# Kernel tuning notes

Measured on AMD Instinct MI355X. Metric: run time of the kernel, lower is better.

Reference implementation:

```python
import jax, jax.numpy as jnp
import numpy as np
from jax import lax

B, C, D, H, W = 2, 64, 64, 96, 96
HID = 8  # max(C // 8, 8)
NEG_SLOPE = 0.01  # torch LeakyReLU default


def setup_inputs() -> dict:
    key = jax.random.key(0)
    k_x, k_dw, k_f1w, k_f1b, k_f2w, k_f2b = jax.random.split(key, 6)
    x = jax.random.normal(k_x, (B, C, D, H, W), dtype=jnp.float32)
    # depthwise 3x3x3 kernel, OIDHW with I = C/groups = 1
    dw_w = jax.random.normal(k_dw, (C, 1, 3, 3, 3), dtype=jnp.float32) * 0.2
    fc1_w = jax.random.normal(k_f1w, (HID, C), dtype=jnp.float32) * 0.1
    fc1_b = jax.random.normal(k_f1b, (HID,), dtype=jnp.float32) * 0.1
    fc2_w = jax.random.normal(k_f2w, (C, HID), dtype=jnp.float32) * 0.1
    fc2_b = jax.random.normal(k_f2b, (C,), dtype=jnp.float32) * 0.1
    return {"x": x, "dw_w": dw_w, "fc1_w": fc1_w, "fc1_b": fc1_b,
            "fc2_w": fc2_w, "fc2_b": fc2_b}


def reference(x, dw_w, fc1_w, fc1_b, fc2_w, fc2_b):
    # depthwise 3x3x3 conv, padding=1, groups=C
    s = lax.conv_general_dilated(
        x, dw_w,
        window_strides=(1, 1, 1),
        padding=[(1, 1), (1, 1), (1, 1)],
        dimension_numbers=("NCDHW", "OIDHW", "NCDHW"),
        feature_group_count=C,
    )
    # squeeze: global average pool over D,H,W -> [B, C]
    z = s.mean(axis=(2, 3, 4))
    # excitation MLP (1x1x1 convs on [B,C,1,1,1] == dense layers on [B,C])
    h = jnp.einsum("bc,hc->bh", z, fc1_w) + fc1_b
    h = jnp.where(h >= 0, h, NEG_SLOPE * h)  # LeakyReLU(0.01)
    w = jax.nn.sigmoid(jnp.einsum("bh,ch->bc", h, fc2_w) + fc2_b)
    # broadcast channel gate
    return x * w[:, :, None, None, None]
```

## Files before the change

### kernel.cpp

```cpp
#include <hip/hip_runtime.h>
#include <math.h>

#define B 2
#define C 64
#define DD 64
#define HH 96
#define WW 96
#define HID 8
#define BC (B * C)
#define SLICE (HH * WW)
#define SLICE4 (SLICE / 4)
#define CHAN (DD * SLICE)
#define CHAN4 (CHAN / 4)
#define ROW4 (WW / 4)

#define RED_BX 16
#define DPB (DD / RED_BX)
#define SC_F4 16
#define SC_BX (CHAN4 / (256 * SC_F4))

#define WS_PART 0
#define WS_GATE (BC * RED_BX)

typedef float f4 __attribute__((ext_vector_type(4)));

__device__ __forceinline__ void compute_clsw(const float* __restrict__ dw_w,
                                             int c, int tid, float* w27) {
    if (tid < 27) {
        int cd = tid / 9, r = tid % 9, ch = r / 3, cw = r % 3;
        int kd0 = (cd == 2) ? 1 : 0, kd1 = (cd == 0) ? 1 : 2;
        int kh0 = (ch == 2) ? 1 : 0, kh1 = (ch == 0) ? 1 : 2;
        int kw0 = (cw == 2) ? 1 : 0, kw1 = (cw == 0) ? 1 : 2;
        float s = 0.f;
        for (int kd = kd0; kd <= kd1; ++kd)
            for (int kh = kh0; kh <= kh1; ++kh)
                for (int kw = kw0; kw <= kw1; ++kw)
                    s += dw_w[c * 27 + kd * 9 + kh * 3 + kw];
        w27[tid] = s;
    }
}

__global__ __launch_bounds__(256) void reduce_kernel(const float* __restrict__ x,
                                                     const float* __restrict__ dw_w,
                                                     float* __restrict__ ws) {
    const int bc = blockIdx.y;
    const int c  = bc & (C - 1);
    const int d0 = blockIdx.x * DPB;
    const int tid = threadIdx.x;

    __shared__ float w27[27];
    __shared__ float part[4];

    compute_clsw(dw_w, c, tid, w27);
    __syncthreads();

    const f4* xb = (const f4*)x + (size_t)bc * CHAN4;
    float acc = 0.f;

    const int h0 = tid / ROW4;
    const int j0 = tid - h0 * ROW4;

    for (int sd = 0; sd < DPB; ++sd) {
        const int d  = d0 + sd;
        const float* w9 = &w27[((d == 0) ? 0 : ((d == DD - 1) ? 2 : 1)) * 9];
        const f4* x4 = xb + (size_t)d * SLICE4;
        int h = h0, j = j0;
        #pragma unroll
        for (int it = 0; it < SLICE4 / 256; ++it) {
            f4 v = x4[it * 256 + tid];
            int chc = (h == 0) ? 0 : ((h == HH - 1) ? 2 : 1);
            float wmid = w9[chc * 3 + 1];
            float w0 = (j == 0) ? w9[chc * 3 + 0] : wmid;
            float w3 = (j == ROW4 - 1) ? w9[chc * 3 + 2] : wmid;
            acc += v.x * w0 + (v.y + v.z) * wmid + v.w * w3;
            h += 10; j += 16;
            if (j >= ROW4) { j -= ROW4; h += 1; }
        }
    }

    for (int off = 32; off > 0; off >>= 1)
        acc += __shfl_down(acc, off, 64);
    if ((tid & 63) == 0) part[tid >> 6] = acc;
    __syncthreads();
    if (tid == 0)
        ws[WS_PART + bc * RED_BX + blockIdx.x] = part[0] + part[1] + part[2] + part[3];
}

__global__ void gate_kernel(const float* __restrict__ fc1_w, const float* __restrict__ fc1_b,
                            const float* __restrict__ fc2_w, const float* __restrict__ fc2_b,
                            float* __restrict__ ws) {
    __shared__ float zsh[BC];
    __shared__ float hsh[B * HID];
    int t = threadIdx.x;
    float s0 = 0.f;
    for (int p = 0; p < RED_BX; ++p) s0 += ws[WS_PART + t * RED_BX + p];
    zsh[t] = s0 * (1.0f / (float)CHAN);
    __syncthreads();
    if (t < B * HID) {
        int b = t >> 3, j = t & 7;
        float s = fc1_b[j];
        for (int cc = 0; cc < C; ++cc) s += fc1_w[j * C + cc] * zsh[b * C + cc];
        hsh[t] = (s >= 0.f) ? s : 0.01f * s;
    }
    __syncthreads();
    int b = t >> 6, cc = t & (C - 1);
    float s = fc2_b[cc];
    for (int j = 0; j < HID; ++j) s += fc2_w[cc * HID + j] * hsh[b * HID + j];
    ws[WS_GATE + t] = 1.f / (1.f + expf(-s));
}

__global__ __launch_bounds__(256) void scale_kernel(const float* __restrict__ x,
                                                    const float* __restrict__ ws,
                                                    float* __restrict__ out) {
    const int bc = (BC - 1) - blockIdx.y;
    const int bx = (SC_BX - 1) - blockIdx.x;
    const float g = ws[WS_GATE + bc];
    const size_t base = (size_t)bc * CHAN4 + (size_t)bx * (256 * SC_F4) + threadIdx.x;
    const f4* xp = (const f4*)x;
    f4* op = (f4*)out;
    #pragma unroll
    for (int k = 0; k < SC_F4; ++k) {
        size_t idx = base + (size_t)k * 256;
        op[idx] = xp[idx] * g;
    }
}

extern "C" void kernel_launch(void* const* d_in, const int* in_sizes, int n_in,
                              void* d_out, int out_size, void* d_ws, size_t ws_size,
                              hipStream_t stream) {
    const float* x     = (const float*)d_in[0];
    const float* dw_w  = (const float*)d_in[1];
    const float* fc1_w = (const float*)d_in[2];
    const float* fc1_b = (const float*)d_in[3];
    const float* fc2_w = (const float*)d_in[4];
    const float* fc2_b = (const float*)d_in[5];
    float* out = (float*)d_out;
    float* ws  = (float*)d_ws;

    reduce_kernel<<<dim3(RED_BX, BC), dim3(256), 0, stream>>>(x, dw_w, ws);
    gate_kernel<<<dim3(1), dim3(BC), 0, stream>>>(fc1_w, fc1_b, fc2_w, fc2_b, ws);
    scale_kernel<<<dim3(SC_BX, BC), dim3(256), 0, stream>>>(x, ws, out);
}
```

Before: 558.0 us.

## Fuse gate MLP into scale kernel and restructure reduction loop for interior chunks

Removes the separate single-block gate kernel. Each scale block now recomputes the channel's gate from the partial sums, which saves one launch and the serialization gap between kernels. The reduction kernel gains a fast path for interior depth chunks: per-position weights are precomputed once and reused across four depth slices, with four independent accumulators to raise memory-level parallelism. The trade-off is redundant MLP work in every scale block, plus the dropped reversed block ordering that previously aimed for cache reuse of x.

```diff
diff --git a/kernel.cpp b/kernel.cpp
--- a/kernel.cpp
+++ b/kernel.cpp
@@ -13,6 +13,7 @@
 #define CHAN (DD * SLICE)
 #define CHAN4 (CHAN / 4)
 #define ROW4 (WW / 4)
+#define SEGS (SLICE4 / 256)
 
 #define RED_BX 16
 #define DPB (DD / RED_BX)
@@ -20,7 +21,6 @@
 #define SC_BX (CHAN4 / (256 * SC_F4))
 
 #define WS_PART 0
-#define WS_GATE (BC * RED_BX)
 
 typedef float f4 __attribute__((ext_vector_type(4)));
 
@@ -43,79 +43,110 @@
 __global__ __launch_bounds__(256) void reduce_kernel(const float* __restrict__ x,
                                                      const float* __restrict__ dw_w,
                                                      float* __restrict__ ws) {
-    const int bc = blockIdx.y;
-    const int c  = bc & (C - 1);
-    const int d0 = blockIdx.x * DPB;
-    const int tid = threadIdx.x;
+    const int bc    = blockIdx.y;
+    const int c     = bc & (C - 1);
+    const int chunk = blockIdx.x;
+    const int d0    = chunk * DPB;
+    const int tid   = threadIdx.x;
 
     __shared__ float w27[27];
     __shared__ float part[4];
-
     compute_clsw(dw_w, c, tid, w27);
     __syncthreads();
 
-    const f4* xb = (const f4*)x + (size_t)bc * CHAN4;
-    float acc = 0.f;
+    const f4* xb = (const f4*)x + (size_t)bc * CHAN4 + (size_t)d0 * SLICE4;
+    float acc[DPB] = {0.f, 0.f, 0.f, 0.f};
 
-    const int h0 = tid / ROW4;
-    const int j0 = tid - h0 * ROW4;
-
-    for (int sd = 0; sd < DPB; ++sd) {
-        const int d  = d0 + sd;
-        const float* w9 = &w27[((d == 0) ? 0 : ((d == DD - 1) ? 2 : 1)) * 9];
-        const f4* x4 = xb + (size_t)d * SLICE4;
-        int h = h0, j = j0;
+    if (chunk != 0 && chunk != RED_BX - 1) {
+        float w0r[SEGS], wmr[SEGS], w3r[SEGS];
         #pragma unroll
-        for (int it = 0; it < SLICE4 / 256; ++it) {
-            f4 v = x4[it * 256 + tid];
+        for (int s = 0; s < SEGS; ++s) {
+            int p = s * 256 + tid;
+            int h = p / ROW4;
+            int j = p - h * ROW4;
             int chc = (h == 0) ? 0 : ((h == HH - 1) ? 2 : 1);
-            float wmid = w9[chc * 3 + 1];
-            float w0 = (j == 0) ? w9[chc * 3 + 0] : wmid;
-            float w3 = (j == ROW4 - 1) ? w9[chc * 3 + 2] : wmid;
-            acc += v.x * w0 + (v.y + v.z) * wmid + v.w * w3;
-            h += 10; j += 16;
-            if (j >= ROW4) { j -= ROW4; h += 1; }
+            float wm = w27[9 + chc * 3 + 1];
+            wmr[s] = wm;
+            w0r[s] = (j == 0)        ? w27[9 + chc * 3 + 0] : wm;
+            w3r[s] = (j == ROW4 - 1) ? w27[9 + chc * 3 + 2] : wm;
+        }
+        #pragma unroll
+        for (int s = 0; s < SEGS; ++s) {
+            const int p = s * 256 + tid;
+            #pragma unroll
+            for (int sd = 0; sd < DPB; ++sd) {
+                f4 v = xb[(size_t)sd * SLICE4 + p];
+                acc[sd] += v.x * w0r[s] + (v.y + v.z) * wmr[s] + v.w * w3r[s];
+            }
+        }
+    } else {
+        #pragma unroll
+        for (int sd = 0; sd < DPB; ++sd) {
+            const int d  = d0 + sd;
+            const int cd = (d == 0) ? 0 : ((d == DD - 1) ? 2 : 1);
+            #pragma unroll
+            for (int s = 0; s < SEGS; ++s) {
+                int p = s * 256 + tid;
+                int h = p / ROW4;
+                int j = p - h * ROW4;
+                int chc = (h == 0) ? 0 : ((h == HH - 1) ? 2 : 1);
+                float wm = w27[cd * 9 + chc * 3 + 1];
+                float w0 = (j == 0)        ? w27[cd * 9 + chc * 3 + 0] : wm;
+                float w3 = (j == ROW4 - 1) ? w27[cd * 9 + chc * 3 + 2] : wm;
+                f4 v = xb[(size_t)sd * SLICE4 + p];
+                acc[sd] += v.x * w0 + (v.y + v.z) * wm + v.w * w3;
+            }
         }
     }
 
+    float a = (acc[0] + acc[1]) + (acc[2] + acc[3]);
     for (int off = 32; off > 0; off >>= 1)
-        acc += __shfl_down(acc, off, 64);
-    if ((tid & 63) == 0) part[tid >> 6] = acc;
+        a += __shfl_down(a, off, 64);
+    if ((tid & 63) == 0) part[tid >> 6] = a;
     __syncthreads();
     if (tid == 0)
-        ws[WS_PART + bc * RED_BX + blockIdx.x] = part[0] + part[1] + part[2] + part[3];
+        ws[WS_PART + bc * RED_BX + chunk] = (part[0] + part[1]) + (part[2] + part[3]);
 }
 
-__global__ void gate_kernel(const float* __restrict__ fc1_w, const float* __restrict__ fc1_b,
-                            const float* __restrict__ fc2_w, const float* __restrict__ fc2_b,
-                            float* __restrict__ ws) {
-    __shared__ float zsh[BC];
-    __shared__ float hsh[B * HID];
-    int t = threadIdx.x;
-    float s0 = 0.f;
-    for (int p = 0; p < RED_BX; ++p) s0 += ws[WS_PART + t * RED_BX + p];
-    zsh[t] = s0 * (1.0f / (float)CHAN);
+__global__ __launch_bounds__(256) void scale_kernel(
+        const float* __restrict__ x,
+        const float* __restrict__ fc1_w, const float* __restrict__ fc1_b,
+        const float* __restrict__ fc2_w, const float* __restrict__ fc2_b,
+        const float* __restrict__ ws, float* __restrict__ out) {
+    const int bc = blockIdx.y;
+    const int b  = bc >> 6;
+    const int c  = bc & (C - 1);
+    const int t  = threadIdx.x;
+
+    __shared__ float zsh[C];
+    __shared__ float hsh[HID];
+    __shared__ float gsh;
+
+    if (t < C) {
+        float s0 = 0.f;
+        #pragma unroll
+        for (int p = 0; p < RED_BX; ++p)
+            s0 += ws[WS_PART + (b * C + t) * RED_BX + p];
+        zsh[t] = s0 * (1.0f / (float)CHAN);
+    }
     __syncthreads();
-    if (t < B * HID) {
-        int b = t >> 3, j = t & 7;
-        float s = fc1_b[j];
-        for (int cc = 0; cc < C; ++cc) s += fc1_w[j * C + cc] * zsh[b * C + cc];
+    if (t < HID) {
+        float s = fc1_b[t];
+        #pragma unroll
+        for (int cc = 0; cc < C; ++cc) s += fc1_w[t * C + cc] * zsh[cc];
         hsh[t] = (s >= 0.f) ? s : 0.01f * s;
     }
     __syncthreads();
-    int b = t >> 6, cc = t & (C - 1);
-    float s = fc2_b[cc];
-    for (int j = 0; j < HID; ++j) s += fc2_w[cc * HID + j] * hsh[b * HID + j];
-    ws[WS_GATE + t] = 1.f / (1.f + expf(-s));
-}
+    if (t == 0) {
+        float s = fc2_b[c];
+        #pragma unroll
+        for (int j = 0; j < HID; ++j) s += fc2_w[c * HID + j] * hsh[j];
+        gsh = 1.f / (1.f + expf(-s));
+    }
+    __syncthreads();
+    const float g = gsh;
 
-__global__ __launch_bounds__(256) void scale_kernel(const float* __restrict__ x,
-                                                    const float* __restrict__ ws,
-                                                    float* __restrict__ out) {
-    const int bc = (BC - 1) - blockIdx.y;
-    const int bx = (SC_BX - 1) - blockIdx.x;
-    const float g = ws[WS_GATE + bc];
-    const size_t base = (size_t)bc * CHAN4 + (size_t)bx * (256 * SC_F4) + threadIdx.x;
+    const size_t base = (size_t)bc * CHAN4 + (size_t)blockIdx.x * (256 * SC_F4) + t;
     const f4* xp = (const f4*)x;
     f4* op = (f4*)out;
     #pragma unroll
@@ -138,6 +169,6 @@
     float* ws  = (float*)d_ws;
 
     reduce_kernel<<<dim3(RED_BX, BC), dim3(256), 0, stream>>>(x, dw_w, ws);
-    gate_kernel<<<dim3(1), dim3(BC), 0, stream>>>(fc1_w, fc1_b, fc2_w, fc2_b, ws);
-    scale_kernel<<<dim3(SC_BX, BC), dim3(256), 0, stream>>>(x, ws, out);
+    scale_kernel<<<dim3(SC_BX, BC), dim3(256), 0, stream>>>(x, fc1_w, fc1_b,
+                                                            fc2_w, fc2_b, ws, out);
 }
```

Measured after the change: 557.5 us. No clear change (-0.1%).
